# Performance work log

Measured on AMD Instinct MI355X. Metric: run time of the kernel, lower is better.

The kernel has to match this reference:

```python
import jax, jax.numpy as jnp
import numpy as np
import math

B, N, C_IN, C_OUT, K, M, DIM = 8, 8192, 64, 128, 16, 16, 3


def setup_inputs() -> dict:
    key = jax.random.key(0)
    ks = jax.random.split(key, 12)
    features = jax.random.normal(ks[0], (B, N, C_IN), dtype=jnp.float32)
    input_pts = jax.random.uniform(ks[1], (B, N, DIM), dtype=jnp.float32)
    output_pts = jax.random.uniform(ks[2], (B, N, DIM), dtype=jnp.float32)
    indices = jax.random.randint(ks[3], (B, N, K), 0, N)
    # main conv weight [C_in, M, C_out], uniform(-bound, bound) as in torch init
    bound = math.sqrt(3.0) * math.sqrt(2.0 / (C_IN + C_OUT))
    weight = jax.random.uniform(ks[4], (C_IN, M, C_OUT), minval=-bound, maxval=bound, dtype=jnp.float32)
    bias = jnp.zeros((C_OUT,), dtype=jnp.float32)
    # kernel element centers inside unit ball [dim, M]
    centers = jax.random.uniform(ks[5], (DIM, M), minval=-1.0, maxval=1.0, dtype=jnp.float32) * 0.57
    # MLP: l1 (dim*M -> 2M), l2 (2M -> M), l3 (M -> M); torch Linear layout [out, in]
    def lin(k, fan_in, fan_out):
        lim = 1.0 / math.sqrt(fan_in)
        kw, kb = jax.random.split(k)
        w = jax.random.uniform(kw, (fan_out, fan_in), minval=-lim, maxval=lim, dtype=jnp.float32)
        b = jax.random.uniform(kb, (fan_out,), minval=-lim, maxval=lim, dtype=jnp.float32)
        return w, b
    l1_w, l1_b = lin(ks[6], DIM * M, 2 * M)
    l2_w, l2_b = lin(ks[7], 2 * M, M)
    l3_w, l3_b = lin(ks[8], M, M)
    return {"features": features, "input_pts": input_pts, "output_pts": output_pts,
            "indices": indices, "centers": centers, "weight": weight, "bias": bias,
            "l1_w": l1_w, "l1_b": l1_b, "l2_w": l2_w, "l2_b": l2_b, "l3_w": l3_w, "l3_b": l3_b}


def _gather(x, idx):
    # x: [B, N, D], idx: [B, No, K] -> [B, No, K, D]
    b, no, k = idx.shape
    flat = jnp.take_along_axis(x, idx.reshape(b, no * k, 1), axis=1)
    return flat.reshape(b, no, k, x.shape[-1])


def reference(features, input_pts, output_pts, indices, centers, weight, bias,
              l1_w, l1_b, l2_w, l2_b, l3_w, l3_b):
    # Gather neighbor features and points
    feats_nb = _gather(features, indices)            # [B, No, K, C_in]
    pts = _gather(input_pts, indices)                # [B, No, K, dim]
    pts = pts - output_pts[:, :, None, :]            # relative coords
    # distances to kernel centers: [B, No, K, dim, M] -> [B, No, K, dim*M]
    d = pts[..., :, None] - centers                  # centers [dim, M]
    d = d.reshape(d.shape[0], d.shape[1], d.shape[2], -1)
    # 3-layer MLP with relu
    d = jax.nn.relu(d @ l1_w.T + l1_b)
    d = jax.nn.relu(d @ l2_w.T + l2_b)
    d = jax.nn.relu(d @ l3_w.T + l3_b)               # [B, No, K, M]
    # weighted neighbor aggregation: contract over K neighbors
    agg = jnp.einsum('bnkc,bnkm->bncm', feats_nb, d)  # [B, No, C_in, M]
    bsz, no = agg.shape[0], agg.shape[1]
    agg = agg.reshape(bsz, no, -1)                    # [B, No, C_in*M]
    out = agg @ weight.reshape(-1, weight.shape[-1])  # [B, No, C_out]
    out = out / feats_nb.shape[2]                     # divide by K
    out = out + bias
    return (out, output_pts)
```

## Files before the change

kernel.cpp:

```cpp
#include <hip/hip_runtime.h>

#define BATCH 8
#define NPTS  8192
#define CIN   64
#define COUT  128
#define KNN   16
#define MD    16
#define PTS   16
#define PTSC  32
#define DT_STR 264
#define AGG_STRIDE 1032

#define NWT    (COUT * CIN * MD)
#define NFBF   (BATCH * NPTS * CIN)
#define NPTS_G (BATCH * NPTS)

typedef __attribute__((ext_vector_type(8))) short short8;
typedef __attribute__((ext_vector_type(4))) short short4v;
typedef __attribute__((ext_vector_type(4))) float f32x4;
typedef __attribute__((ext_vector_type(2))) float f32x2;

__device__ __forceinline__ short f2bf(float f) {
  unsigned u = __float_as_uint(f);
  u = (u + 0x7fffu + ((u >> 16) & 1u)) >> 16;
  return (short)u;
}

__global__ __launch_bounds__(256) void prep_kernel(
    const float* __restrict__ weight, const float* __restrict__ opts,
    const float* __restrict__ feats, const float* __restrict__ centers,
    const float* __restrict__ l1_w, const float* __restrict__ l1_b,
    const float* __restrict__ l2_w, const float* __restrict__ l3_w,
    short* __restrict__ Wt, short* __restrict__ fbf,
    short* __restrict__ l2bf, short* __restrict__ l3bf, float* __restrict__ Gc4,
    float* __restrict__ out_tail, int mode) {
  int tid = blockIdx.x * 256 + threadIdx.x;
  if (mode >= 1 && tid < NWT) {
    int co, o;
    if (mode == 3) {
      int j = tid & 7, quad = (tid >> 3) & 3, lrow = (tid >> 5) & 15;
      int kb = (tid >> 9) & 31, wv = tid >> 14;
      co = wv * 16 + lrow;
      o = kb * 32 + quad * 8 + j;
    } else {
      co = tid >> 10;
      o = tid & 1023;
    }
    int k;
    if (mode == 3) {
      int r = o & 3, q = (o >> 2) & 3, m = (o >> 4) & 15, ct = o >> 8;
      k = ct * 256 + q * 64 + r * 16 + m;
    } else {
      k = o;
    }
    Wt[tid] = f2bf(weight[(size_t)k * COUT + co]);
  }
  if (mode >= 2 && tid < NFBF / 4) {
    int row = tid >> 4, lr = tid & 15;
    const float* fr = feats + ((size_t)row << 6) + lr;
    short4v v = {f2bf(fr[0]), f2bf(fr[16]), f2bf(fr[32]), f2bf(fr[48])};
    *(short4v*)(fbf + ((size_t)row << 6) + lr * 4) = v;
  }
  if (mode == 3) {
    if (tid < 512) l2bf[tid] = f2bf(l2_w[tid]);
    if (tid < 256) l3bf[tid] = f2bf(l3_w[tid]);
    if (tid < 32) {
      float g0 = 0.f, g1 = 0.f, g2 = 0.f, cc = l1_b[tid];
      const float* wr = l1_w + tid * 48;
#pragma unroll
      for (int m = 0; m < 16; ++m) { g0 += wr[m]; g1 += wr[16 + m]; g2 += wr[32 + m]; }
#pragma unroll
      for (int i = 0; i < 48; ++i) cc -= wr[i] * centers[i];
      Gc4[tid * 4 + 0] = g0; Gc4[tid * 4 + 1] = g1; Gc4[tid * 4 + 2] = g2; Gc4[tid * 4 + 3] = cc;
    }
  }
  if (tid < BATCH * NPTS * 3) out_tail[tid] = opts[tid];
}

__global__ __launch_bounds__(512, 4) void conv_kernel(
    const int* __restrict__ indices, const short* __restrict__ fbf,
    const short* __restrict__ Wt, const short* __restrict__ l2bf,
    const short* __restrict__ l3bf, const float* __restrict__ Gc4,
    const float* __restrict__ l2_b, const float* __restrict__ l3_b,
    const float* __restrict__ input_pts, const float* __restrict__ output_pts,
    const float* __restrict__ bias, float* __restrict__ out) {
  __shared__ __align__(16) short s_agg[PTSC * AGG_STRIDE];

  const int t = threadIdx.x, blk = blockIdx.x;
  const int w = ((blk & 7) << 8) | (blk >> 3);
  const int batch = w >> 8, n0 = (w & 255) * PTSC;
  const int lane = t & 63, wv = t >> 6, quad = lane >> 4, lrow = lane & 15;
  const size_t bbase = (size_t)batch * NPTS;

  const int myid = indices[(bbase + n0) * KNN + t];
  const float* op = output_pts + (bbase + n0 + wv * 4 + quad) * 3;
  const float* ip = input_pts + (bbase + myid) * 3;
  const float px = ip[0] - op[0], py = ip[1] - op[1], pz = ip[2] - op[2];

  f32x4 G[8];
#pragma unroll
  for (int j = 0; j < 8; ++j) G[j] = *(const f32x4*)(Gc4 + (quad * 8 + j) * 4);
  const short8  w2f = *(const short8*)(l2bf + lrow * 32 + quad * 8);
  const short4v w3f = *(const short4v*)(l3bf + lrow * 16 + quad * 4);
  const f32x4 b2f = *(const f32x4*)(l2_b + quad * 4);
  const float b3v = l3_b[lrow];
  const f32x4 b3f = {b3v, b3v, b3v, b3v};

  short4v g[4][4];
#pragma unroll
  for (int pp = 0; pp < 4; ++pp)
#pragma unroll
    for (int j = 0; j < 4; ++j) {
      const int idn = __shfl(myid, pp * 16 + quad * 4 + j);
      g[pp][j] = *(const short4v*)(fbf + ((bbase + idn) << 6) + lrow * 4);
    }

  short8 h1f[4];
#pragma unroll
  for (int pp = 0; pp < 4; ++pp) {
    const float qx = __shfl(px, pp * 16 + lrow);
    const float qy = __shfl(py, pp * 16 + lrow);
    const float qz = __shfl(pz, pp * 16 + lrow);
#pragma unroll
    for (int j = 0; j < 8; ++j) {
      const f32x4 Gx = G[j];
      h1f[pp][j] = f2bf(fmaxf(fmaf(Gx[0], qx, fmaf(Gx[1], qy, fmaf(Gx[2], qz, Gx[3]))), 0.f));
    }
  }

  f32x4 h2[4];
#pragma unroll
  for (int pp = 0; pp < 4; ++pp)
    h2[pp] = __builtin_amdgcn_mfma_f32_16x16x32_bf16(w2f, h1f[pp], b2f, 0, 0, 0);
  short4v h2f[4];
#pragma unroll
  for (int pp = 0; pp < 4; ++pp)
#pragma unroll
    for (int r = 0; r < 4; ++r) h2f[pp][r] = f2bf(fmaxf(h2[pp][r], 0.f));

  f32x4 h3[4];
#pragma unroll
  for (int pp = 0; pp < 4; ++pp)
    h3[pp] = __builtin_amdgcn_mfma_f32_16x16x16bf16_1k(h2f[pp], w3f, b3f, 0, 0, 0);
  short4v dfr[4];
#pragma unroll
  for (int pp = 0; pp < 4; ++pp)
#pragma unroll
    for (int r = 0; r < 4; ++r) dfr[pp][r] = f2bf(fmaxf(h3[pp][r], 0.f) * 0.0625f);

#pragma unroll
  for (int pp = 0; pp < 4; ++pp) {
    const int pt = wv * 4 + pp;
    const short4v g0 = g[pp][0], g1 = g[pp][1], g2 = g[pp][2], g3 = g[pp][3];
#pragma unroll
    for (int ct = 0; ct < 4; ++ct) {
      const short4v afr = {g0[ct], g1[ct], g2[ct], g3[ct]};
      const f32x4 dd = __builtin_amdgcn_mfma_f32_16x16x16bf16_1k(
          afr, dfr[pp], (f32x4){0.f, 0.f, 0.f, 0.f}, 0, 0, 0);
      short4v sv;
#pragma unroll
      for (int r = 0; r < 4; ++r) sv[r] = f2bf(dd[r]);
      *(short4v*)&s_agg[pt * AGG_STRIDE + ct * 256 + lrow * 16 + quad * 4] = sv;
    }
  }

  const int co = wv * 16 + lrow;
  const short* wp = Wt + wv * 16384 + lrow * 32 + quad * 8;
  short8 Bpf[4];
#pragma unroll
  for (int i = 0; i < 4; ++i) Bpf[i] = *(const short8*)(wp + i * 512);

  asm volatile("s_waitcnt lgkmcnt(0)" ::: "memory");
  __builtin_amdgcn_s_barrier();
  asm volatile("" ::: "memory");

  f32x4 acc0 = {0.f, 0.f, 0.f, 0.f};
  f32x4 acc1 = {0.f, 0.f, 0.f, 0.f};
  const short* a0 = s_agg + lrow * AGG_STRIDE + quad * 8;
  const short* a1 = a0 + 16 * AGG_STRIDE;
#pragma unroll
  for (int kb = 0; kb < 32; ++kb) {
    const short8 bfr = Bpf[kb & 3];
    if (kb < 28) Bpf[kb & 3] = *(const short8*)(wp + (kb + 4) * 512);
    const short8 av0 = *(const short8*)(a0 + kb * 32);
    const short8 av1 = *(const short8*)(a1 + kb * 32);
    acc0 = __builtin_amdgcn_mfma_f32_16x16x32_bf16(av0, bfr, acc0, 0, 0, 0);
    acc1 = __builtin_amdgcn_mfma_f32_16x16x32_bf16(av1, bfr, acc1, 0, 0, 0);
  }
  const float bi = bias[co];
#pragma unroll
  for (int r = 0; r < 4; ++r) {
    const int p0 = quad * 4 + r;
    out[(bbase + n0 + p0) * COUT + co] = acc0[r] + bi;
    out[(bbase + n0 + 16 + p0) * COUT + co] = acc1[r] + bi;
  }
}

template <int MODE>
__global__ __launch_bounds__(256, 3) void ptconv_mono(
    const float* __restrict__ features, const float* __restrict__ input_pts,
    const float* __restrict__ output_pts, const int* __restrict__ indices,
    const float* __restrict__ centers, const float* __restrict__ weight,
    const float* __restrict__ bias,
    const float* __restrict__ l1_w, const float* __restrict__ l1_b,
    const float* __restrict__ l2_w, const float* __restrict__ l2_b,
    const float* __restrict__ l3_w, const float* __restrict__ l3_b,
    const short* __restrict__ Wt, const short* __restrict__ fbf,
    float* __restrict__ out) {
  __shared__ __align__(16) short s_dT[MD * DT_STR];
  __shared__ __align__(16) short s_agg[PTS * AGG_STRIDE];
  __shared__ __align__(16) int   s_idx[PTS * KNN];

  const int t = threadIdx.x;
  const int blk = blockIdx.x;
  const int batch = blk >> 9;
  const int n0 = (blk & 511) * PTS;
  const int lane = t & 63;
  const int wv = t >> 6;
  const int quad = lane >> 4;
  const int lrow = lane & 15;

  s_idx[t] = indices[((size_t)batch * NPTS + n0) * KNN + t];
  {
    const int pt = t >> 4;
    const int id = s_idx[t];
    const float* op = &output_pts[((size_t)batch * NPTS + n0 + pt) * 3];
    const float* ip = &input_pts[((size_t)batch * NPTS + id) * 3];
    const float px = ip[0] - op[0], py = ip[1] - op[1], pz = ip[2] - op[2];
    f32x2 dv[24];
    {
      const f32x2 px2 = {px, px}, py2 = {py, py}, pz2 = {pz, pz};
      const f32x2* cx = (const f32x2*)centers;
      const f32x2* cy = (const f32x2*)(centers + 16);
      const f32x2* cz = (const f32x2*)(centers + 32);
#pragma unroll
      for (int i = 0; i < 8; ++i) {
        dv[i] = px2 - cx[i]; dv[8 + i] = py2 - cy[i]; dv[16 + i] = pz2 - cz[i];
      }
    }
    float h1[32];
#pragma unroll
    for (int o = 0; o < 32; ++o) {
      const f32x2* wr = (const f32x2*)(l1_w + o * 48);
      f32x2 acc = {0.f, 0.f};
#pragma unroll
      for (int i = 0; i < 24; ++i) acc += dv[i] * wr[i];
      h1[o] = fmaxf(acc[0] + acc[1] + l1_b[o], 0.f);
    }
    f32x2 h1v[16];
#pragma unroll
    for (int i = 0; i < 16; ++i) h1v[i] = (f32x2){h1[2 * i], h1[2 * i + 1]};
    float h2[16];
#pragma unroll
    for (int o = 0; o < 16; ++o) {
      const f32x2* wr = (const f32x2*)(l2_w + o * 32);
      f32x2 acc = {0.f, 0.f};
#pragma unroll
      for (int i = 0; i < 16; ++i) acc += h1v[i] * wr[i];
      h2[o] = fmaxf(acc[0] + acc[1] + l2_b[o], 0.f);
    }
    f32x2 h2v[8];
#pragma unroll
    for (int i = 0; i < 8; ++i) h2v[i] = (f32x2){h2[2 * i], h2[2 * i + 1]};
#pragma unroll
    for (int o = 0; o < 16; ++o) {
      const f32x2* wr = (const f32x2*)(l3_w + o * 16);
      f32x2 acc = {0.f, 0.f};
#pragma unroll
      for (int i = 0; i < 8; ++i) acc += h2v[i] * wr[i];
      s_dT[o * DT_STR + t] = f2bf(fmaxf(acc[0] + acc[1] + l3_b[o], 0.f));
    }
  }
  __syncthreads();
  {
#pragma unroll
    for (int pp = 0; pp < 4; ++pp) {
      const int pt = wv * 4 + pp;
      const short4v bfrag = *(const short4v*)&s_dT[lrow * DT_STR + pt * 16 + quad * 4];
      const int4 idx4 = *(const int4*)&s_idx[pt * 16 + quad * 4];
#pragma unroll
      for (int ct = 0; ct < 4; ++ct) {
        short4v afr;
#pragma unroll
        for (int j = 0; j < 4; ++j) {
          const int id = ((const int*)&idx4)[j];
          const size_t base = ((size_t)batch * NPTS + id) * CIN;
          if (MODE >= 2) afr[j] = fbf[base + lrow * 4 + ct];
          else           afr[j] = f2bf(features[base + ct * 16 + lrow]);
        }
        f32x4 dd = __builtin_amdgcn_mfma_f32_16x16x16bf16_1k(
            afr, bfrag, (f32x4){0.f, 0.f, 0.f, 0.f}, 0, 0, 0);
#pragma unroll
        for (int r = 0; r < 4; ++r) {
          const int rr = (r + quad) & 3;
          const int c = ct * 16 + quad * 4 + rr;
          s_agg[pt * AGG_STRIDE + c * 16 + lrow] = f2bf(dd[rr]);
        }
      }
    }
  }
  __syncthreads();
  {
    f32x4 acc0 = {0.f, 0.f, 0.f, 0.f};
    f32x4 acc1 = {0.f, 0.f, 0.f, 0.f};
    const int co0 = wv * 32 + lrow;
    const int co1 = co0 + 16;
    const short* arow = s_agg + lrow * AGG_STRIDE + quad * 8;
#pragma unroll 4
    for (int kb = 0; kb < 32; ++kb) {
      const short8 a = *(const short8*)(arow + kb * 32);
      short8 b0, b1;
      if (MODE >= 1) {
        b0 = *(const short8*)(Wt + (size_t)co0 * 1024 + kb * 32 + quad * 8);
        b1 = *(const short8*)(Wt + (size_t)co1 * 1024 + kb * 32 + quad * 8);
      } else {
#pragma unroll
        for (int j = 0; j < 8; ++j) {
          const int kk = kb * 32 + quad * 8 + j;
          b0[j] = f2bf(weight[(size_t)kk * COUT + co0]);
          b1[j] = f2bf(weight[(size_t)kk * COUT + co1]);
        }
      }
      acc0 = __builtin_amdgcn_mfma_f32_16x16x32_bf16(a, b0, acc0, 0, 0, 0);
      acc1 = __builtin_amdgcn_mfma_f32_16x16x32_bf16(a, b1, acc1, 0, 0, 0);
    }
    const float bi0 = bias[co0], bi1 = bias[co1];
#pragma unroll
    for (int r = 0; r < 4; ++r) {
      const int pt = quad * 4 + r;
      const size_t rowo = ((size_t)batch * NPTS + n0 + pt) * COUT;
      out[rowo + co0] = acc0[r] * 0.0625f + bi0;
      out[rowo + co1] = acc1[r] * 0.0625f + bi1;
    }
  }
}

extern "C" void kernel_launch(void* const* d_in, const int* in_sizes, int n_in,
                              void* d_out, int out_size, void* d_ws, size_t ws_size,
                              hipStream_t stream) {
  const float* features   = (const float*)d_in[0];
  const float* input_pts  = (const float*)d_in[1];
  const float* output_pts = (const float*)d_in[2];
  const int*   indices    = (const int*)d_in[3];
  const float* centers    = (const float*)d_in[4];
  const float* weight     = (const float*)d_in[5];
  const float* bias       = (const float*)d_in[6];
  const float* l1_w       = (const float*)d_in[7];
  const float* l1_b       = (const float*)d_in[8];
  const float* l2_w       = (const float*)d_in[9];
  const float* l2_b       = (const float*)d_in[10];
  const float* l3_w       = (const float*)d_in[11];
  const float* l3_b       = (const float*)d_in[12];
  float* out = (float*)d_out;

  short* Wt   = (short*)d_ws;
  short* fbf  = Wt + NWT;
  short* l2bf = fbf + NFBF;
  short* l3bf = l2bf + 512;
  float* Gc4  = (float*)(l3bf + 256);
  const size_t need3 = (size_t)(NWT + NFBF + 512 + 256) * 2 + 512;

  int mode = 0;
  if (ws_size >= need3) mode = 3;
  else if (ws_size >= (size_t)(NWT + NFBF) * 2) mode = 2;
  else if (ws_size >= (size_t)NWT * 2) mode = 1;

  float* out_tail = out + (size_t)BATCH * NPTS * COUT;
  const int prep_elems = (mode >= 2) ? (NFBF / 4) : BATCH * NPTS * 3;
  prep_kernel<<<(prep_elems + 255) / 256, 256, 0, stream>>>(
      weight, output_pts, features, centers, l1_w, l1_b, l2_w, l3_w,
      Wt, fbf, l2bf, l3bf, Gc4, out_tail, mode);

  if (mode == 3) {
    conv_kernel<<<NPTS_G / PTSC, 512, 0, stream>>>(
        indices, fbf, Wt, l2bf, l3bf, Gc4, l2_b, l3_b, input_pts, output_pts, bias, out);
  } else if (mode == 2) {
    ptconv_mono<2><<<NPTS_G / PTS, 256, 0, stream>>>(features, input_pts, output_pts, indices,
        centers, weight, bias, l1_w, l1_b, l2_w, l2_b, l3_w, l3_b, Wt, fbf, out);
  } else if (mode == 1) {
    ptconv_mono<1><<<NPTS_G / PTS, 256, 0, stream>>>(features, input_pts, output_pts, indices,
        centers, weight, bias, l1_w, l1_b, l2_w, l2_b, l3_w, l3_b, Wt, fbf, out);
  } else {
    ptconv_mono<0><<<NPTS_G / PTS, 256, 0, stream>>>(features, input_pts, output_pts, indices,
        centers, weight, bias, l1_w, l1_b, l2_w, l2_b, l3_w, l3_b, Wt, fbf, out);
  }
}
```

Measured before the change: 145.2 us.

## Process two 32-point tiles per block, prefetching second tile's gathers during first

Each conv_kernel block now handles 64 output points as two sequential 32-point tiles, halving the grid. The second tile's neighbor indices and feature gathers are issued before the first tile's GEMM so their latency overlaps with compute, and shared memory is reused between tiles with an extra barrier. This trades parallelism (fewer blocks) and higher register pressure for latency hiding of the gathers.

```diff
diff --git a/kernel.cpp b/kernel.cpp
--- a/kernel.cpp
+++ b/kernel.cpp
@@ -87,15 +87,17 @@
   __shared__ __align__(16) short s_agg[PTSC * AGG_STRIDE];
 
   const int t = threadIdx.x, blk = blockIdx.x;
-  const int w = ((blk & 7) << 8) | (blk >> 3);
-  const int batch = w >> 8, n0 = (w & 255) * PTSC;
+  const int w = ((blk & 7) << 7) | (blk >> 3);
+  const int batch = w >> 7, n0 = (w & 127) * 64;
   const int lane = t & 63, wv = t >> 6, quad = lane >> 4, lrow = lane & 15;
   const size_t bbase = (size_t)batch * NPTS;
 
-  const int myid = indices[(bbase + n0) * KNN + t];
-  const float* op = output_pts + (bbase + n0 + wv * 4 + quad) * 3;
-  const float* ip = input_pts + (bbase + myid) * 3;
-  const float px = ip[0] - op[0], py = ip[1] - op[1], pz = ip[2] - op[2];
+  const int myid0 = indices[(bbase + n0) * KNN + t];
+  const int myid1 = indices[(bbase + n0 + 32) * KNN + t];
+
+  const float* op0 = output_pts + (bbase + n0 + wv * 4 + quad) * 3;
+  const float* ip0 = input_pts + (bbase + myid0) * 3;
+  const float px0 = ip0[0] - op0[0], py0 = ip0[1] - op0[1], pz0 = ip0[2] - op0[2];
 
   f32x4 G[8];
 #pragma unroll
@@ -106,66 +108,105 @@
   const float b3v = l3_b[lrow];
   const f32x4 b3f = {b3v, b3v, b3v, b3v};
 
-  short4v g[4][4];
+  short4v ga[4][4];
 #pragma unroll
   for (int pp = 0; pp < 4; ++pp)
 #pragma unroll
     for (int j = 0; j < 4; ++j) {
-      const int idn = __shfl(myid, pp * 16 + quad * 4 + j);
-      g[pp][j] = *(const short4v*)(fbf + ((bbase + idn) << 6) + lrow * 4);
-    }
-
-  short8 h1f[4];
-#pragma unroll
-  for (int pp = 0; pp < 4; ++pp) {
-    const float qx = __shfl(px, pp * 16 + lrow);
-    const float qy = __shfl(py, pp * 16 + lrow);
-    const float qz = __shfl(pz, pp * 16 + lrow);
-#pragma unroll
-    for (int j = 0; j < 8; ++j) {
-      const f32x4 Gx = G[j];
-      h1f[pp][j] = f2bf(fmaxf(fmaf(Gx[0], qx, fmaf(Gx[1], qy, fmaf(Gx[2], qz, Gx[3]))), 0.f));
-    }
-  }
-
-  f32x4 h2[4];
-#pragma unroll
-  for (int pp = 0; pp < 4; ++pp)
-    h2[pp] = __builtin_amdgcn_mfma_f32_16x16x32_bf16(w2f, h1f[pp], b2f, 0, 0, 0);
-  short4v h2f[4];
-#pragma unroll
-  for (int pp = 0; pp < 4; ++pp)
-#pragma unroll
-    for (int r = 0; r < 4; ++r) h2f[pp][r] = f2bf(fmaxf(h2[pp][r], 0.f));
-
-  f32x4 h3[4];
-#pragma unroll
-  for (int pp = 0; pp < 4; ++pp)
-    h3[pp] = __builtin_amdgcn_mfma_f32_16x16x16bf16_1k(h2f[pp], w3f, b3f, 0, 0, 0);
-  short4v dfr[4];
-#pragma unroll
-  for (int pp = 0; pp < 4; ++pp)
-#pragma unroll
-    for (int r = 0; r < 4; ++r) dfr[pp][r] = f2bf(fmaxf(h3[pp][r], 0.f) * 0.0625f);
-
-#pragma unroll
-  for (int pp = 0; pp < 4; ++pp) {
-    const int pt = wv * 4 + pp;
-    const short4v g0 = g[pp][0], g1 = g[pp][1], g2 = g[pp][2], g3 = g[pp][3];
-#pragma unroll
-    for (int ct = 0; ct < 4; ++ct) {
-      const short4v afr = {g0[ct], g1[ct], g2[ct], g3[ct]};
-      const f32x4 dd = __builtin_amdgcn_mfma_f32_16x16x16bf16_1k(
-          afr, dfr[pp], (f32x4){0.f, 0.f, 0.f, 0.f}, 0, 0, 0);
-      short4v sv;
-#pragma unroll
-      for (int r = 0; r < 4; ++r) sv[r] = f2bf(dd[r]);
-      *(short4v*)&s_agg[pt * AGG_STRIDE + ct * 256 + lrow * 16 + quad * 4] = sv;
-    }
-  }
+      const int idn = __shfl(myid0, pp * 16 + quad * 4 + j);
+      ga[pp][j] = *(const short4v*)(fbf + ((bbase + idn) << 6) + lrow * 4);
+    }
+
+  const float* op1 = output_pts + (bbase + n0 + 32 + wv * 4 + quad) * 3;
+  const float* ip1 = input_pts + (bbase + myid1) * 3;
+  const float px1 = ip1[0] - op1[0], py1 = ip1[1] - op1[1], pz1 = ip1[2] - op1[2];
+
+  auto tile_pass = [&](float tpx, float tpy, float tpz, short4v (&gg)[4][4],
+                       const f32x4 (&Gr)[8]) {
+    short8 h1f[4];
+#pragma unroll
+    for (int pp = 0; pp < 4; ++pp) {
+      const float qx = __shfl(tpx, pp * 16 + lrow);
+      const float qy = __shfl(tpy, pp * 16 + lrow);
+      const float qz = __shfl(tpz, pp * 16 + lrow);
+#pragma unroll
+      for (int j = 0; j < 8; ++j) {
+        const f32x4 Gx = Gr[j];
+        h1f[pp][j] = f2bf(fmaxf(fmaf(Gx[0], qx, fmaf(Gx[1], qy, fmaf(Gx[2], qz, Gx[3]))), 0.f));
+      }
+    }
+    f32x4 h2[4];
+#pragma unroll
+    for (int pp = 0; pp < 4; ++pp)
+      h2[pp] = __builtin_amdgcn_mfma_f32_16x16x32_bf16(w2f, h1f[pp], b2f, 0, 0, 0);
+    short4v h2f[4];
+#pragma unroll
+    for (int pp = 0; pp < 4; ++pp)
+#pragma unroll
+      for (int r = 0; r < 4; ++r) h2f[pp][r] = f2bf(fmaxf(h2[pp][r], 0.f));
+    f32x4 h3[4];
+#pragma unroll
+    for (int pp = 0; pp < 4; ++pp)
+      h3[pp] = __builtin_amdgcn_mfma_f32_16x16x16bf16_1k(h2f[pp], w3f, b3f, 0, 0, 0);
+    short4v dfr[4];
+#pragma unroll
+    for (int pp = 0; pp < 4; ++pp)
+#pragma unroll
+      for (int r = 0; r < 4; ++r) dfr[pp][r] = f2bf(fmaxf(h3[pp][r], 0.f) * 0.0625f);
+#pragma unroll
+    for (int pp = 0; pp < 4; ++pp) {
+      const int pt = wv * 4 + pp;
+      const short4v g0 = gg[pp][0], g1 = gg[pp][1], g2 = gg[pp][2], g3 = gg[pp][3];
+#pragma unroll
+      for (int ct = 0; ct < 4; ++ct) {
+        const short4v afr = {g0[ct], g1[ct], g2[ct], g3[ct]};
+        const f32x4 dd = __builtin_amdgcn_mfma_f32_16x16x16bf16_1k(
+            afr, dfr[pp], (f32x4){0.f, 0.f, 0.f, 0.f}, 0, 0, 0);
+        short4v sv;
+#pragma unroll
+        for (int r = 0; r < 4; ++r) sv[r] = f2bf(dd[r]);
+        *(short4v*)&s_agg[pt * AGG_STRIDE + ct * 256 + lrow * 16 + quad * 4] = sv;
+      }
+    }
+  };
 
   const int co = wv * 16 + lrow;
   const short* wp = Wt + wv * 16384 + lrow * 32 + quad * 8;
+  const float bi = bias[co];
+  const short* a0 = s_agg + lrow * AGG_STRIDE + quad * 8;
+  const short* a1 = a0 + 16 * AGG_STRIDE;
+
+  auto gemm_out = [&](short8 (&Bpf)[4], int row0) {
+    f32x4 acc0 = {0.f, 0.f, 0.f, 0.f};
+    f32x4 acc1 = {0.f, 0.f, 0.f, 0.f};
+#pragma unroll
+    for (int kb = 0; kb < 32; ++kb) {
+      const short8 bfr = Bpf[kb & 3];
+      if (kb < 28) Bpf[kb & 3] = *(const short8*)(wp + (kb + 4) * 512);
+      const short8 av0 = *(const short8*)(a0 + kb * 32);
+      const short8 av1 = *(const short8*)(a1 + kb * 32);
+      acc0 = __builtin_amdgcn_mfma_f32_16x16x32_bf16(av0, bfr, acc0, 0, 0, 0);
+      acc1 = __builtin_amdgcn_mfma_f32_16x16x32_bf16(av1, bfr, acc1, 0, 0, 0);
+    }
+#pragma unroll
+    for (int r = 0; r < 4; ++r) {
+      const int p0 = quad * 4 + r;
+      out[(bbase + row0 + p0) * COUT + co] = acc0[r] + bi;
+      out[(bbase + row0 + 16 + p0) * COUT + co] = acc1[r] + bi;
+    }
+  };
+
+  tile_pass(px0, py0, pz0, ga, G);
+
+  short4v gb[4][4];
+#pragma unroll
+  for (int pp = 0; pp < 4; ++pp)
+#pragma unroll
+    for (int j = 0; j < 4; ++j) {
+      const int idn = __shfl(myid1, pp * 16 + quad * 4 + j);
+      gb[pp][j] = *(const short4v*)(fbf + ((bbase + idn) << 6) + lrow * 4);
+    }
+
   short8 Bpf[4];
 #pragma unroll
   for (int i = 0; i < 4; ++i) Bpf[i] = *(const short8*)(wp + i * 512);
@@ -174,26 +215,25 @@
   __builtin_amdgcn_s_barrier();
   asm volatile("" ::: "memory");
 
-  f32x4 acc0 = {0.f, 0.f, 0.f, 0.f};
-  f32x4 acc1 = {0.f, 0.f, 0.f, 0.f};
-  const short* a0 = s_agg + lrow * AGG_STRIDE + quad * 8;
-  const short* a1 = a0 + 16 * AGG_STRIDE;
-#pragma unroll
-  for (int kb = 0; kb < 32; ++kb) {
-    const short8 bfr = Bpf[kb & 3];
-    if (kb < 28) Bpf[kb & 3] = *(const short8*)(wp + (kb + 4) * 512);
-    const short8 av0 = *(const short8*)(a0 + kb * 32);
-    const short8 av1 = *(const short8*)(a1 + kb * 32);
-    acc0 = __builtin_amdgcn_mfma_f32_16x16x32_bf16(av0, bfr, acc0, 0, 0, 0);
-    acc1 = __builtin_amdgcn_mfma_f32_16x16x32_bf16(av1, bfr, acc1, 0, 0, 0);
-  }
-  const float bi = bias[co];
-#pragma unroll
-  for (int r = 0; r < 4; ++r) {
-    const int p0 = quad * 4 + r;
-    out[(bbase + n0 + p0) * COUT + co] = acc0[r] + bi;
-    out[(bbase + n0 + 16 + p0) * COUT + co] = acc1[r] + bi;
-  }
+  gemm_out(Bpf, n0);
+
+  __builtin_amdgcn_s_barrier();
+  asm volatile("" ::: "memory");
+
+  f32x4 G2[8];
+#pragma unroll
+  for (int j = 0; j < 8; ++j) G2[j] = *(const f32x4*)(Gc4 + (quad * 8 + j) * 4);
+
+  tile_pass(px1, py1, pz1, gb, G2);
+
+#pragma unroll
+  for (int i = 0; i < 4; ++i) Bpf[i] = *(const short8*)(wp + i * 512);
+
+  asm volatile("s_waitcnt lgkmcnt(0)" ::: "memory");
+  __builtin_amdgcn_s_barrier();
+  asm volatile("" ::: "memory");
+
+  gemm_out(Bpf, n0 + 32);
 }
 
 template <int MODE>
@@ -372,7 +412,7 @@
       Wt, fbf, l2bf, l3bf, Gc4, out_tail, mode);
 
   if (mode == 3) {
-    conv_kernel<<<NPTS_G / PTSC, 512, 0, stream>>>(
+    conv_kernel<<<NPTS_G / 64, 512, 0, stream>>>(
         indices, fbf, Wt, l2bf, l3bf, Gc4, l2_b, l3_b, input_pts, output_pts, bias, out);
   } else if (mode == 2) {
     ptconv_mono<2><<<NPTS_G / PTS, 256, 0, stream>>>(features, input_pts, output_pts, indices,
```

After: 156.7 us. 1.08x slower.
